# Optimization experiments

Measured on AMD Instinct MI355X. Metric: run time of the kernel, lower is better.

## Reference

```python
import jax, jax.numpy as jnp
import numpy as np

N, E = 50000, 1600000
IN, HID, OUT, H, ED = 128, 16, 40, 4, 16
HC = HID * H  # 64
NEG_SLOPE = 0.2
EPS = 1e-16


def gat_conv(x, src, dst, e_attr, W, att_s, att_d, We, att_e, bias):
    # x: [N, Fin]; src/dst: [E_tot]; e_attr: [E_tot, ED]
    n = x.shape[0]
    h = (x @ W).reshape(n, H, HID)                      # [N,H,C]
    a_s = (h * att_s).sum(-1)                           # [N,H]
    a_d = (h * att_d).sum(-1)                           # [N,H]
    ee = (e_attr @ We).reshape(-1, H, HID)              # [E,H,C]
    a_e = (ee * att_e).sum(-1)                          # [E,H]
    alpha = a_s[src] + a_d[dst] + a_e                   # [E,H]
    alpha = jax.nn.leaky_relu(alpha, NEG_SLOPE)
    amax = jax.ops.segment_max(alpha, dst, num_segments=n)
    ex = jnp.exp(alpha - amax[dst])
    den = jax.ops.segment_sum(ex, dst, num_segments=n)
    alpha = ex / (den[dst] + EPS)
    msg = h[src] * alpha[..., None]                     # [E,H,C]
    out = jax.ops.segment_sum(msg, dst, num_segments=n) # [N,H,C]
    return out.reshape(n, HC) + bias


def setup_inputs() -> dict:
    key = jax.random.key(0)
    ks = jax.random.split(key, 20)
    s = 0.05
    inp = {
        "x": jax.random.normal(ks[0], (N, IN), jnp.float32),
        "edge_index": jax.random.randint(ks[1], (2, E), 0, N, jnp.int64 if jax.config.jax_enable_x64 else jnp.int32),
        "edge_attr": jax.random.normal(ks[2], (E, ED), jnp.float32),
        # conv1
        "W1": jax.random.normal(ks[3], (IN, HC)) * s,
        "att_src1": jax.random.normal(ks[4], (H, HID)) * s,
        "att_dst1": jax.random.normal(ks[5], (H, HID)) * s,
        "We1": jax.random.normal(ks[6], (ED, HC)) * s,
        "att_e1": jax.random.normal(ks[7], (H, HID)) * s,
        "b1": jnp.zeros((HC,), jnp.float32),
        # conv2
        "W2": jax.random.normal(ks[8], (HC, HC)) * s,
        "att_src2": jax.random.normal(ks[9], (H, HID)) * s,
        "att_dst2": jax.random.normal(ks[10], (H, HID)) * s,
        "We2": jax.random.normal(ks[11], (ED, HC)) * s,
        "att_e2": jax.random.normal(ks[12], (H, HID)) * s,
        "b2": jnp.zeros((HC,), jnp.float32),
        # head
        "lw1": jax.random.normal(ks[13], (HC, HID)) * s,
        "lb1": jnp.zeros((HID,), jnp.float32),
        "lw2": jax.random.normal(ks[14], (HID, OUT)) * s,
        "lb2": jnp.zeros((OUT,), jnp.float32),
    }
    return inp


def reference(x, edge_index, edge_attr,
              W1, att_src1, att_dst1, We1, att_e1, b1,
              W2, att_src2, att_dst2, We2, att_e2, b2,
              lw1, lb1, lw2, lb2):
    n = x.shape[0]
    loop = jnp.arange(n, dtype=edge_index.dtype)
    src = jnp.concatenate([edge_index[0], loop])
    dst = jnp.concatenate([edge_index[1], loop])
    # self-loop edge_attr filled with mean over edges (PyG fill_value='mean')
    mean_attr = edge_attr.mean(axis=0, keepdims=True)
    ea = jnp.concatenate([edge_attr, jnp.broadcast_to(mean_attr, (n, edge_attr.shape[1]))])

    h = gat_conv(x, src, dst, ea, W1, att_src1, att_dst1, We1, att_e1, b1)
    h = jax.nn.relu(h)  # dropout is identity at eval
    h = gat_conv(h, src, dst, ea, W2, att_src2, att_dst2, We2, att_e2, b2)
    h = jax.nn.relu(h)
    h = (h @ lw1 + lb1) @ lw2 + lb2  # Linear -> Dropout(eval) -> Linear
    return jax.nn.log_softmax(h, axis=1)
```

## Files before the change

kernel.cpp:

```cpp
#include <hip/hip_runtime.h>
#include <hip/hip_fp16.h>

#define N_NODES 50000
#define E_EDGES 1600000
#define NEG 0.2f
#define EDGE_BLOCKS 6250
#define RED_BLOCKS 64
#define SCAN_BLOCKS ((N_NODES + 255)/256)
#define HBLK 128
#define EPHB (E_EDGES/HBLK)
#define NPAIR (N_NODES/2)
#define NODE_BLOCKS 2048

__device__ __forceinline__ float lrelu(float x){ return fmaxf(x, NEG*x); }
__device__ __forceinline__ float bcastlane(float v, int k){
    return __int_as_float(__builtin_amdgcn_readlane(__float_as_int(v), k));
}
__device__ __forceinline__ unsigned bf16rn(float x){
    unsigned u = __float_as_uint(x);
    return (u + 0x7FFFu + ((u >> 16) & 1u)) >> 16;
}
__device__ __forceinline__ float bf2f(unsigned short u){
    return __uint_as_float(((unsigned)u) << 16);
}
__device__ __forceinline__ unsigned h16(float x){
    return (unsigned)__half_as_ushort(__float2half(x));
}
__device__ __forceinline__ float f16dec(unsigned u){
    return __half2float(__ushort_as_half((unsigned short)(u & 0xFFFFu)));
}

#if __has_builtin(__builtin_amdgcn_cvt_f32_fp8) && __has_builtin(__builtin_amdgcn_cvt_pk_fp8_f32)
__device__ __forceinline__ unsigned enc8(float x){
    return (unsigned)__builtin_amdgcn_cvt_pk_fp8_f32(x, x, 0, false) & 0xFFu;
}
__device__ __forceinline__ float dec8(unsigned b){
    return __builtin_amdgcn_cvt_f32_fp8((int)b, 0);
}
#else
__device__ __forceinline__ unsigned enc8(float x){
    float ax = fabsf(x); unsigned s = (x < 0.f) ? 0x80u : 0u;
    if (ax < 0.015625f){
        int q = (int)rintf(ax * 512.f);
        return s | (unsigned)q;
    }
    if (ax >= 448.f) return s | 0x7Eu;
    int ee; float mm = frexpf(ax, &ee);
    int q = (int)rintf(mm * 16.f);
    int E = ee + 6;
    if (q == 16){ q = 8; ++E; }
    if (E > 15){ return s | 0x7Eu; }
    return s | ((unsigned)E << 3) | (unsigned)(q - 8);
}
__device__ __forceinline__ float dec8(unsigned b){
    unsigned s = b >> 7, e = (b >> 3) & 15u, m = b & 7u;
    float mag = e ? __uint_as_float(((e + 120u) << 23) | (m << 20))
                  : (float)m * 0.001953125f;
    return s ? -mag : mag;
}
#endif


__global__ void k_prep1(const float* __restrict__ We1, const float* __restrict__ atte1,
                        const float* __restrict__ We2, const float* __restrict__ atte2,
                        float* __restrict__ small){
    int t = threadIdx.x;
    int k = t >> 2, hh = t & 3;
    float w1 = 0.f, w2 = 0.f;
    for (int c = 0; c < 16; ++c){
        w1 = fmaf(We1[k*64 + hh*16 + c], atte1[hh*16 + c], w1);
        w2 = fmaf(We2[k*64 + hh*16 + c], atte2[hh*16 + c], w2);
    }
    small[32 + t] = w1;
    small[96 + t] = w2;
}

__global__ __launch_bounds__(256) void k_hist1(const int* __restrict__ dst,
                                               unsigned* __restrict__ bhist,
                                               unsigned short* __restrict__ lrank){
    extern __shared__ unsigned hist[];
    for (int i = threadIdx.x; i < NPAIR; i += 256) hist[i] = 0u;
    __syncthreads();
    int b0 = blockIdx.x*EPHB;
    for (int i = threadIdx.x; i < EPHB; i += 256){
        int e = b0 + i;
        int d = dst[e];
        unsigned sh = (unsigned)(d & 1) * 16u;
        unsigned old = atomicAdd(&hist[d >> 1], 1u << sh);
        lrank[e] = (unsigned short)((old >> sh) & 0xFFFFu);
    }
    __syncthreads();
    unsigned* bh = bhist + (size_t)blockIdx.x*NPAIR;
    for (int i = threadIdx.x; i < NPAIR; i += 256) bh[i] = hist[i];
}

__global__ __launch_bounds__(256) void k_hist2(const unsigned* __restrict__ bhist,
                                               unsigned* __restrict__ boff,
                                               int* __restrict__ deg){
    int j = blockIdx.x*256 + threadIdx.x;
    if (j >= NPAIR) return;
    unsigned lo = 0, hi = 0;
    for (int b = 0; b < HBLK; ++b){
        unsigned v = bhist[(size_t)b*NPAIR + j];
        boff[(size_t)b*NPAIR + j] = lo | (hi << 16);
        lo += v & 0xFFFFu;
        hi += v >> 16;
    }
    deg[2*j]     = (int)lo;
    deg[2*j + 1] = (int)hi;
}

__global__ __launch_bounds__(256) void k_scan_a(const int* __restrict__ deg, int* __restrict__ bsum){
    int i = blockIdx.x*256 + threadIdx.x;
    int v = (i < N_NODES) ? deg[i] : 0;
    v += __shfl_xor(v,1); v += __shfl_xor(v,2); v += __shfl_xor(v,4);
    v += __shfl_xor(v,8); v += __shfl_xor(v,16); v += __shfl_xor(v,32);
    __shared__ int ws[4];
    if ((threadIdx.x & 63) == 0) ws[threadIdx.x >> 6] = v;
    __syncthreads();
    if (threadIdx.x == 0) bsum[blockIdx.x] = ws[0] + ws[1] + ws[2] + ws[3];
}

__global__ __launch_bounds__(256) void k_scan_b(const int* __restrict__ bsum, int* __restrict__ boff){
    __shared__ int sm[256];
    int t = threadIdx.x;
    int v = (t < SCAN_BLOCKS) ? bsum[t] : 0;
    sm[t] = v;
    __syncthreads();
    for (int off = 1; off < 256; off <<= 1){
        int u = (t >= off) ? sm[t-off] : 0;
        __syncthreads();
        sm[t] += u;
        __syncthreads();
    }
    boff[t] = (t > 0) ? sm[t-1] : 0;
    if (t == 0) boff[SCAN_BLOCKS] = sm[255];
}

__global__ __launch_bounds__(256) void k_scan_c(const int* __restrict__ deg, const int* __restrict__ boff,
                                                int* __restrict__ base){
    int i = blockIdx.x*256 + threadIdx.x;
    int lane = threadIdx.x & 63, wid = threadIdx.x >> 6;
    int v = (i < N_NODES) ? deg[i] : 0;
    int inc = v;
    for (int off = 1; off < 64; off <<= 1){
        int u = __shfl_up(inc, off);
        if (lane >= off) inc += u;
    }
    __shared__ int wsum[4];
    if (lane == 63) wsum[wid] = inc;
    __syncthreads();
    int wpre = 0;
#pragma unroll
    for (int w = 0; w < 4; ++w) wpre += (w < wid) ? wsum[w] : 0;
    int ex = boff[blockIdx.x] + wpre + inc - v;
    if (i < N_NODES) base[i] = ex;
    if (i == N_NODES - 1) base[N_NODES] = ex + v;
}

template<int FIN>
__global__ __launch_bounds__(256) void k_node(const float* __restrict__ in, const float* __restrict__ W,
                                              const float* __restrict__ att_s, const float* __restrict__ att_d,
                                              unsigned char* __restrict__ hb8,
                                              unsigned short* __restrict__ a_s,
                                              unsigned short* __restrict__ a_d){
    __shared__ float Wl[FIN*64];
    for (int i = threadIdx.x; i < FIN*64; i += 256) Wl[i] = W[i];
    __syncthreads();
    int lane = threadIdx.x & 63;
    int wid  = threadIdx.x >> 6;
    for (int nb = blockIdx.x*4; nb < N_NODES; nb += NODE_BLOCKS*4){
        int node = nb + wid;
        const float* row = in + (size_t)node*FIN;
        float x0 = row[lane];
        float x1 = 0.f;
        if constexpr (FIN == 128) x1 = row[64 + lane];
        float acc = 0.f;
#pragma unroll
        for (int k = 0; k < 64; ++k)
            acc = fmaf(bcastlane(x0, k), Wl[k*64 + lane], acc);
        if constexpr (FIN == 128){
#pragma unroll
            for (int k = 0; k < 64; ++k)
                acc = fmaf(bcastlane(x1, k), Wl[(64+k)*64 + lane], acc);
        }
        hb8[(size_t)node*64 + lane] = (unsigned char)enc8(acc);
        float ps = acc * att_s[lane];
        float pd = acc * att_d[lane];
        ps += __shfl_xor(ps,1); ps += __shfl_xor(ps,2); ps += __shfl_xor(ps,4); ps += __shfl_xor(ps,8);
        pd += __shfl_xor(pd,1); pd += __shfl_xor(pd,2); pd += __shfl_xor(pd,4); pd += __shfl_xor(pd,8);
        if ((lane & 15) == 0){
            a_s[node*4 + (lane>>4)] = (unsigned short)bf16rn(ps);
            a_d[node*4 + (lane>>4)] = (unsigned short)bf16rn(pd);
        }
    }
}

__global__ __launch_bounds__(256) void k_edges(const int* __restrict__ src, const int* __restrict__ dst,
                                               const unsigned short* __restrict__ lrank,
                                               const unsigned* __restrict__ boff32,
                                               const float* __restrict__ ea, const float* __restrict__ small,
                                               const int* __restrict__ base, uint4* __restrict__ rec,
                                               float* __restrict__ partials){
    __shared__ float w1[64], w2[64];
    __shared__ float red[64];
    if (threadIdx.x < 64){ w1[threadIdx.x] = small[32+threadIdx.x]; w2[threadIdx.x] = small[96+threadIdx.x]; }
    __syncthreads();
    int e = blockIdx.x*256 + threadIdx.x;
    int s = src[e], d = dst[e];
    int hb = e / EPHB;
    unsigned offpk = boff32[(size_t)hb*NPAIR + (d >> 1)];
    int p = base[d] + (int)((offpk >> ((unsigned)(d & 1)*16u)) & 0xFFFFu) + (int)lrank[e];
    const float4* eap = (const float4*)(ea + (size_t)e*16);
    float cs[16];
    float ae1[4] = {0,0,0,0}, ae2[4] = {0,0,0,0};
#pragma unroll
    for (int q = 0; q < 4; ++q){
        float4 v4 = eap[q];
        float vv[4] = {v4.x, v4.y, v4.z, v4.w};
#pragma unroll
        for (int r = 0; r < 4; ++r){
            int k = q*4 + r;
            float xv = vv[r];
            cs[k] = xv;
#pragma unroll
            for (int hh = 0; hh < 4; ++hh){
                ae1[hh] = fmaf(xv, w1[k*4+hh], ae1[hh]);
                ae2[hh] = fmaf(xv, w2[k*4+hh], ae2[hh]);
            }
        }
    }
    unsigned q8[4];
#pragma unroll
    for (int hh = 0; hh < 4; ++hh){
        int qv = (int)rintf(ae2[hh]*256.f) + 128;
        qv = qv < 0 ? 0 : (qv > 255 ? 255 : qv);
        q8[hh] = (unsigned)qv;
    }
    uint4 r;
    r.x = (unsigned)s;
    r.y = h16(ae1[0]) | (h16(ae1[1]) << 16);
    r.z = h16(ae1[2]) | (h16(ae1[3]) << 16);
    r.w = q8[0] | (q8[1] << 8) | (q8[2] << 16) | (q8[3] << 24);
    rec[p] = r;
#pragma unroll
    for (int k = 0; k < 16; ++k){
        float v = cs[k];
        v += __shfl_xor(v,1); v += __shfl_xor(v,2); v += __shfl_xor(v,4);
        v += __shfl_xor(v,8); v += __shfl_xor(v,16); v += __shfl_xor(v,32);
        if ((threadIdx.x & 63) == 0) red[k*4 + (threadIdx.x>>6)] = v;
    }
    __syncthreads();
    if (threadIdx.x < 16){
        float v = red[threadIdx.x*4] + red[threadIdx.x*4+1] + red[threadIdx.x*4+2] + red[threadIdx.x*4+3];
        partials[blockIdx.x*16 + threadIdx.x] = v;
    }
}

__global__ __launch_bounds__(256) void k_red(const float* __restrict__ partials, float* __restrict__ red16){
    const int TOT = EDGE_BLOCKS*16;
    int t = threadIdx.x;
    float v = 0.f;
    for (int idx = blockIdx.x*256 + t; idx < TOT; idx += RED_BLOCKS*256) v += partials[idx];
    v += __shfl_xor(v,16); v += __shfl_xor(v,32);
    __shared__ float sm[64];
    int lane = t & 63, wid = t >> 6;
    if (lane < 16) sm[wid*16 + lane] = v;
    __syncthreads();
    if (t < 16) red16[blockIdx.x*16 + t] = sm[t] + sm[16+t] + sm[32+t] + sm[48+t];
}

__global__ __launch_bounds__(256) void k_prep2(float* __restrict__ small, const float* __restrict__ red16){
    __shared__ float sm[256];
    __shared__ float mean_s[16];
    int t = threadIdx.x;
    float v = 0.f;
    for (int r = (t>>4); r < RED_BLOCKS; r += 16) v += red16[r*16 + (t&15)];
    sm[t] = v;
    __syncthreads();
    if (t < 16){
        float s = 0.f;
#pragma unroll
        for (int i = 0; i < 16; ++i) s += sm[t + 16*i];
        float m = s * (1.0f/(float)E_EDGES);
        mean_s[t] = m; small[16+t] = m;
    }
    __syncthreads();
    if (t < 4){
        float a1 = 0.f, a2 = 0.f;
#pragma unroll
        for (int k = 0; k < 16; ++k){
            a1 = fmaf(mean_s[k], small[32 + k*4 + t], a1);
            a2 = fmaf(mean_s[k], small[96 + k*4 + t], a2);
        }
        small[160+t] = a1; small[164+t] = a2;
    }
}

template<int L>
__device__ __forceinline__ float ae_of(const uint4& r, int h4){
    if constexpr (L == 1){
        return f16dec(((h4 < 2) ? r.y : r.z) >> ((h4 & 1)*16));
    } else {
        return (float)((int)((r.w >> (h4*8)) & 255u) - 128) * 0.00390625f;
    }
}

template<int L>
__global__ __launch_bounds__(256) void k_agg(const uint4* __restrict__ recs, const int* __restrict__ base,
                                             const unsigned char* __restrict__ hb8,
                                             const unsigned short* __restrict__ a_s,
                                             const unsigned short* __restrict__ a_d,
                                             const float* __restrict__ aeloop, const float* __restrict__ bias,
                                             float* __restrict__ out){
    int lane = threadIdx.x & 63;
    int n = blockIdx.x*4 + (threadIdx.x >> 6);
    int hh = lane >> 4;
    int e16 = lane >> 2, h4 = lane & 3;
    float ad_acc = bf2f(a_d[n*4+hh]);
    float ad_w   = bf2f(a_d[n*4+h4]);
    float wL = __expf(lrelu(bf2f(a_s[n*4+hh]) + ad_acc + aeloop[hh]));
    float s0 = wL, s1 = 0.f, s2 = 0.f, s3 = 0.f;
    float acc0 = wL * dec8(hb8[(unsigned)n*64u + (unsigned)lane]);
    float acc1 = 0.f, acc2 = 0.f, acc3 = 0.f;
    int b0 = base[n], b1 = base[n+1];
    for (int pc = b0; pc < b1; pc += 32){
        int remA = b1 - pc;       int mA = remA < 16 ? remA : 16;
        int remB = b1 - pc - 16;  int mB = remB < 0 ? 0 : (remB < 16 ? remB : 16);
        float wa = 0.f, wb = 0.f;
        unsigned sia = 0u, sib = 0u;
        if (e16 < mA){
            uint4 r = recs[pc + e16];
            sia = r.x;
            wa = __expf(lrelu(bf2f(a_s[sia*4u + (unsigned)h4]) + ad_w + ae_of<L>(r, h4)));
        }
        if (e16 < mB){
            uint4 r = recs[pc + 16 + e16];
            sib = r.x;
            wb = __expf(lrelu(bf2f(a_s[sib*4u + (unsigned)h4]) + ad_w + ae_of<L>(r, h4)));
        }
        if (mA == 16){
#pragma unroll
            for (int j = 0; j < 16; j += 2){
                unsigned siA = (unsigned)__shfl((int)sia, j*4);
                unsigned siB = (unsigned)__shfl((int)sia, j*4 + 4);
                float wA = __shfl(wa, j*4 + hh);
                float wB = __shfl(wa, j*4 + 4 + hh);
                float hvA = dec8(hb8[siA*64u + (unsigned)lane]);
                float hvB = dec8(hb8[siB*64u + (unsigned)lane]);
                s0 += wA; acc0 = fmaf(wA, hvA, acc0);
                s1 += wB; acc1 = fmaf(wB, hvB, acc1);
            }
        } else {
            int j = 0;
            for (; j + 2 <= mA; j += 2){
                unsigned siA = (unsigned)__shfl((int)sia, j*4);
                unsigned siB = (unsigned)__shfl((int)sia, j*4 + 4);
                float wA = __shfl(wa, j*4 + hh);
                float wB = __shfl(wa, j*4 + 4 + hh);
                float hvA = dec8(hb8[siA*64u + (unsigned)lane]);
                float hvB = dec8(hb8[siB*64u + (unsigned)lane]);
                s0 += wA; acc0 = fmaf(wA, hvA, acc0);
                s1 += wB; acc1 = fmaf(wB, hvB, acc1);
            }
            if (j < mA){
                unsigned si = (unsigned)__shfl((int)sia, j*4);
                float wj = __shfl(wa, j*4 + hh);
                float hv = dec8(hb8[si*64u + (unsigned)lane]);
                s0 += wj; acc0 = fmaf(wj, hv, acc0);
            }
        }
        if (mB == 16){
#pragma unroll
            for (int j = 0; j < 16; j += 2){
                unsigned siA = (unsigned)__shfl((int)sib, j*4);
                unsigned siB = (unsigned)__shfl((int)sib, j*4 + 4);
                float wA = __shfl(wb, j*4 + hh);
                float wB = __shfl(wb, j*4 + 4 + hh);
                float hvA = dec8(hb8[siA*64u + (unsigned)lane]);
                float hvB = dec8(hb8[siB*64u + (unsigned)lane]);
                s2 += wA; acc2 = fmaf(wA, hvA, acc2);
                s3 += wB; acc3 = fmaf(wB, hvB, acc3);
            }
        } else if (mB > 0){
            int j = 0;
            for (; j + 2 <= mB; j += 2){
                unsigned siA = (unsigned)__shfl((int)sib, j*4);
                unsigned siB = (unsigned)__shfl((int)sib, j*4 + 4);
                float wA = __shfl(wb, j*4 + hh);
                float wB = __shfl(wb, j*4 + 4 + hh);
                float hvA = dec8(hb8[siA*64u + (unsigned)lane]);
                float hvB = dec8(hb8[siB*64u + (unsigned)lane]);
                s2 += wA; acc2 = fmaf(wA, hvA, acc2);
                s3 += wB; acc3 = fmaf(wB, hvB, acc3);
            }
            if (j < mB){
                unsigned si = (unsigned)__shfl((int)sib, j*4);
                float wj = __shfl(wb, j*4 + hh);
                float hv = dec8(hb8[si*64u + (unsigned)lane]);
                s2 += wj; acc2 = fmaf(wj, hv, acc2);
            }
        }
    }
    float s = (s0 + s1) + (s2 + s3);
    float val = ((acc0 + acc1) + (acc2 + acc3)) / (s + 1e-16f) + bias[lane];
    out[(size_t)n*64 + lane] = fmaxf(val, 0.f);
}

__global__ __launch_bounds__(256) void k_head(const float* __restrict__ h2,
                                              const float* __restrict__ lw1, const float* __restrict__ lb1,
                                              const float* __restrict__ lw2, const float* __restrict__ lb2,
                                              float* __restrict__ out){
    int n = blockIdx.x*256 + threadIdx.x;
    if (n >= N_NODES) return;
    float y16[16];
#pragma unroll
    for (int j = 0; j < 16; ++j) y16[j] = lb1[j];
    const float4* hp = (const float4*)(h2 + (size_t)n*64);
#pragma unroll
    for (int k4 = 0; k4 < 16; ++k4){
        float4 hv = hp[k4];
        float hvv[4] = {hv.x, hv.y, hv.z, hv.w};
#pragma unroll
        for (int r = 0; r < 4; ++r){
            float x = hvv[r];
            int k = k4*4 + r;
#pragma unroll
            for (int j = 0; j < 16; ++j) y16[j] = fmaf(x, lw1[k*16+j], y16[j]);
        }
    }
    float y[40];
#pragma unroll
    for (int o = 0; o < 40; ++o) y[o] = lb2[o];
#pragma unroll
    for (int j = 0; j < 16; ++j){
        float x = y16[j];
#pragma unroll
        for (int o = 0; o < 40; ++o) y[o] = fmaf(x, lw2[j*40+o], y[o]);
    }
    float mx = y[0];
#pragma unroll
    for (int o = 1; o < 40; ++o) mx = fmaxf(mx, y[o]);
    float sum = 0.f;
#pragma unroll
    for (int o = 0; o < 40; ++o) sum += __expf(y[o] - mx);
    float ls = __logf(sum) + mx;
    float* op = out + (size_t)n*40;
#pragma unroll
    for (int o = 0; o < 40; ++o) op[o] = y[o] - ls;
}

extern "C" void kernel_launch(void* const* d_in, const int* in_sizes, int n_in,
                              void* d_out, int out_size, void* d_ws, size_t ws_size,
                              hipStream_t stream){
    const float* x     = (const float*)d_in[0];
    const int*   ei    = (const int*)  d_in[1];
    const float* ea    = (const float*)d_in[2];
    const float* W1    = (const float*)d_in[3];
    const float* atts1 = (const float*)d_in[4];
    const float* attd1 = (const float*)d_in[5];
    const float* We1   = (const float*)d_in[6];
    const float* atte1 = (const float*)d_in[7];
    const float* b1    = (const float*)d_in[8];
    const float* W2    = (const float*)d_in[9];
    const float* atts2 = (const float*)d_in[10];
    const float* attd2 = (const float*)d_in[11];
    const float* We2   = (const float*)d_in[12];
    const float* atte2 = (const float*)d_in[13];
    const float* b2    = (const float*)d_in[14];
    const float* lw1   = (const float*)d_in[15];
    const float* lb1   = (const float*)d_in[16];
    const float* lw2   = (const float*)d_in[17];
    const float* lb2   = (const float*)d_in[18];
    float* outp = (float*)d_out;

    const int* srcp = ei;
    const int* dstp = ei + E_EDGES;

    char* ws = (char*)d_ws;
    size_t off = 0;
    auto alloc = [&](size_t bytes) -> void* {
        void* p = ws + off;
        off = (off + bytes + 255) & ~(size_t)255;
        return p;
    };
    float*  smallf   = (float*) alloc(256*sizeof(float));
    float*  partials = (float*) alloc((size_t)EDGE_BLOCKS*16*sizeof(float));
    float*  red16    = (float*) alloc((size_t)RED_BLOCKS*16*sizeof(float));
    int*    deg      = (int*)   alloc((size_t)N_NODES*sizeof(int));
    int*    base     = (int*)   alloc((size_t)(N_NODES+1)*sizeof(int));
    int*    bsum     = (int*)   alloc((size_t)(SCAN_BLOCKS+1)*sizeof(int));
    int*    boffs    = (int*)   alloc((size_t)(SCAN_BLOCKS+1)*sizeof(int));
    unsigned short* lrank = (unsigned short*)alloc((size_t)E_EDGES*sizeof(unsigned short));
    unsigned* bhist  = (unsigned*)alloc((size_t)HBLK*NPAIR*sizeof(unsigned));
    unsigned* boff32 = (unsigned*)alloc((size_t)HBLK*NPAIR*sizeof(unsigned));
    uint4*  rec      = (uint4*) alloc((size_t)E_EDGES*16);
    unsigned char* hb8 = (unsigned char*)alloc((size_t)N_NODES*64);
    float*  obuf     = (float*) alloc((size_t)N_NODES*64*sizeof(float));
    unsigned short* asb = (unsigned short*)alloc((size_t)N_NODES*4*sizeof(unsigned short));
    unsigned short* adb = (unsigned short*)alloc((size_t)N_NODES*4*sizeof(unsigned short));

    const int NB = N_NODES/4;
    const int HB = (N_NODES + 255)/256;
    const int PB = (NPAIR + 255)/256;

    k_prep1<<<1, 64, 0, stream>>>(We1, atte1, We2, atte2, smallf);
    k_hist1<<<HBLK, 256, NPAIR*sizeof(unsigned), stream>>>(dstp, bhist, lrank);
    k_hist2<<<PB, 256, 0, stream>>>(bhist, boff32, deg);
    k_scan_a<<<SCAN_BLOCKS, 256, 0, stream>>>(deg, bsum);
    k_scan_b<<<1, 256, 0, stream>>>(bsum, boffs);
    k_scan_c<<<SCAN_BLOCKS, 256, 0, stream>>>(deg, boffs, base);

    k_node<128><<<NODE_BLOCKS, 256, 0, stream>>>(x, W1, atts1, attd1, hb8, asb, adb);
    k_edges<<<EDGE_BLOCKS, 256, 0, stream>>>(srcp, dstp, lrank, boff32, ea, smallf,
                                             base, rec, partials);
    k_red<<<RED_BLOCKS, 256, 0, stream>>>(partials, red16);
    k_prep2<<<1, 256, 0, stream>>>(smallf, red16);
    k_agg<1><<<NB, 256, 0, stream>>>(rec, base, hb8, asb, adb, smallf + 160, b1, obuf);

    k_node<64><<<NODE_BLOCKS, 256, 0, stream>>>(obuf, W2, atts2, attd2, hb8, asb, adb);
    k_agg<2><<<NB, 256, 0, stream>>>(rec, base, hb8, asb, adb, smallf + 164, b2, obuf);

    k_head<<<HB, 256, 0, stream>>>(obuf, lw1, lb1, lw2, lb2, outp);
}
```

Before: 280.8 us.

## Fuse layer-2 node transform into agg1 and MLP head into agg2

The first aggregation kernel now computes the layer-2 linear projection and attention scores per node directly, using W2 staged in shared memory. The second aggregation fuses the head MLP and log-softmax, so the fp32 intermediate buffer and two extra launches go away. Both kernels switch to a fixed 2048-block grid-stride loop, which changes occupancy and scheduling. The edge-kernel reduction is also changed to reduce over 16-lane groups with a 256-entry shared buffer.

```diff
diff --git a/kernel.cpp b/kernel.cpp
--- a/kernel.cpp
+++ b/kernel.cpp
@@ -203,7 +203,7 @@
                                                const int* __restrict__ base, uint4* __restrict__ rec,
                                                float* __restrict__ partials){
     __shared__ float w1[64], w2[64];
-    __shared__ float red[64];
+    __shared__ float red[256];
     if (threadIdx.x < 64){ w1[threadIdx.x] = small[32+threadIdx.x]; w2[threadIdx.x] = small[96+threadIdx.x]; }
     __syncthreads();
     int e = blockIdx.x*256 + threadIdx.x;
@@ -246,13 +246,14 @@
 #pragma unroll
     for (int k = 0; k < 16; ++k){
         float v = cs[k];
-        v += __shfl_xor(v,1); v += __shfl_xor(v,2); v += __shfl_xor(v,4);
-        v += __shfl_xor(v,8); v += __shfl_xor(v,16); v += __shfl_xor(v,32);
-        if ((threadIdx.x & 63) == 0) red[k*4 + (threadIdx.x>>6)] = v;
+        v += __shfl_xor(v,1); v += __shfl_xor(v,2); v += __shfl_xor(v,4); v += __shfl_xor(v,8);
+        if ((threadIdx.x & 15) == k) red[k*16 + (threadIdx.x >> 4)] = v;
     }
     __syncthreads();
     if (threadIdx.x < 16){
-        float v = red[threadIdx.x*4] + red[threadIdx.x*4+1] + red[threadIdx.x*4+2] + red[threadIdx.x*4+3];
+        float v = 0.f;
+#pragma unroll
+        for (int g = 0; g < 16; ++g) v += red[threadIdx.x*16 + g];
         partials[blockIdx.x*16 + threadIdx.x] = v;
     }
 }
@@ -307,14 +308,13 @@
 }
 
 template<int L>
-__global__ __launch_bounds__(256) void k_agg(const uint4* __restrict__ recs, const int* __restrict__ base,
-                                             const unsigned char* __restrict__ hb8,
-                                             const unsigned short* __restrict__ a_s,
-                                             const unsigned short* __restrict__ a_d,
-                                             const float* __restrict__ aeloop, const float* __restrict__ bias,
-                                             float* __restrict__ out){
-    int lane = threadIdx.x & 63;
-    int n = blockIdx.x*4 + (threadIdx.x >> 6);
+__device__ __forceinline__ float agg_node(int n, int lane, const uint4* __restrict__ recs,
+                                          const int* __restrict__ base,
+                                          const unsigned char* __restrict__ hb8,
+                                          const unsigned short* __restrict__ a_s,
+                                          const unsigned short* __restrict__ a_d,
+                                          const float* __restrict__ aeloop,
+                                          const float* __restrict__ bias){
     int hh = lane >> 4;
     int e16 = lane >> 2, h4 = lane & 3;
     float ad_acc = bf2f(a_d[n*4+hh]);
@@ -404,50 +404,85 @@
     }
     float s = (s0 + s1) + (s2 + s3);
     float val = ((acc0 + acc1) + (acc2 + acc3)) / (s + 1e-16f) + bias[lane];
-    out[(size_t)n*64 + lane] = fmaxf(val, 0.f);
-}
-
-__global__ __launch_bounds__(256) void k_head(const float* __restrict__ h2,
+    return fmaxf(val, 0.f);
+}
+
+__global__ __launch_bounds__(256) void k_agg1(const uint4* __restrict__ recs, const int* __restrict__ base,
+                                              const unsigned char* __restrict__ hb8a,
+                                              const unsigned short* __restrict__ as1,
+                                              const unsigned short* __restrict__ ad1,
+                                              const float* __restrict__ aeloop, const float* __restrict__ b1,
+                                              const float* __restrict__ W2,
+                                              const float* __restrict__ atts2, const float* __restrict__ attd2,
+                                              unsigned char* __restrict__ hb8b,
+                                              unsigned short* __restrict__ as2,
+                                              unsigned short* __restrict__ ad2){
+    __shared__ float Wl[64*64];
+    for (int i = threadIdx.x; i < 64*64; i += 256) Wl[i] = W2[i];
+    __syncthreads();
+    int lane = threadIdx.x & 63;
+    int wid  = threadIdx.x >> 6;
+    for (int n0 = blockIdx.x*4; n0 < N_NODES; n0 += NODE_BLOCKS*4){
+        int n = n0 + wid;
+        float val = agg_node<1>(n, lane, recs, base, hb8a, as1, ad1, aeloop, b1);
+        float acc = 0.f;
+#pragma unroll
+        for (int k = 0; k < 64; ++k)
+            acc = fmaf(bcastlane(val, k), Wl[k*64 + lane], acc);
+        hb8b[(size_t)n*64 + lane] = (unsigned char)enc8(acc);
+        float ps = acc * atts2[lane];
+        float pd = acc * attd2[lane];
+        ps += __shfl_xor(ps,1); ps += __shfl_xor(ps,2); ps += __shfl_xor(ps,4); ps += __shfl_xor(ps,8);
+        pd += __shfl_xor(pd,1); pd += __shfl_xor(pd,2); pd += __shfl_xor(pd,4); pd += __shfl_xor(pd,8);
+        if ((lane & 15) == 0){
+            as2[n*4 + (lane>>4)] = (unsigned short)bf16rn(ps);
+            ad2[n*4 + (lane>>4)] = (unsigned short)bf16rn(pd);
+        }
+    }
+}
+
+__global__ __launch_bounds__(256) void k_agg2(const uint4* __restrict__ recs, const int* __restrict__ base,
+                                              const unsigned char* __restrict__ hb8b,
+                                              const unsigned short* __restrict__ as2,
+                                              const unsigned short* __restrict__ ad2,
+                                              const float* __restrict__ aeloop, const float* __restrict__ b2,
                                               const float* __restrict__ lw1, const float* __restrict__ lb1,
                                               const float* __restrict__ lw2, const float* __restrict__ lb2,
                                               float* __restrict__ out){
-    int n = blockIdx.x*256 + threadIdx.x;
-    if (n >= N_NODES) return;
-    float y16[16];
-#pragma unroll
-    for (int j = 0; j < 16; ++j) y16[j] = lb1[j];
-    const float4* hp = (const float4*)(h2 + (size_t)n*64);
-#pragma unroll
-    for (int k4 = 0; k4 < 16; ++k4){
-        float4 hv = hp[k4];
-        float hvv[4] = {hv.x, hv.y, hv.z, hv.w};
-#pragma unroll
-        for (int r = 0; r < 4; ++r){
-            float x = hvv[r];
-            int k = k4*4 + r;
-#pragma unroll
-            for (int j = 0; j < 16; ++j) y16[j] = fmaf(x, lw1[k*16+j], y16[j]);
-        }
-    }
-    float y[40];
-#pragma unroll
-    for (int o = 0; o < 40; ++o) y[o] = lb2[o];
-#pragma unroll
-    for (int j = 0; j < 16; ++j){
-        float x = y16[j];
-#pragma unroll
-        for (int o = 0; o < 40; ++o) y[o] = fmaf(x, lw2[j*40+o], y[o]);
-    }
-    float mx = y[0];
-#pragma unroll
-    for (int o = 1; o < 40; ++o) mx = fmaxf(mx, y[o]);
-    float sum = 0.f;
-#pragma unroll
-    for (int o = 0; o < 40; ++o) sum += __expf(y[o] - mx);
-    float ls = __logf(sum) + mx;
-    float* op = out + (size_t)n*40;
-#pragma unroll
-    for (int o = 0; o < 40; ++o) op[o] = y[o] - ls;
+    __shared__ float lw1s[64*16];
+    __shared__ float lw2s[16*40];
+    __shared__ float hsh[4][64];
+    __shared__ float ysh[4][16];
+    for (int i = threadIdx.x; i < 64*16; i += 256) lw1s[i] = lw1[i];
+    for (int i = threadIdx.x; i < 16*40; i += 256) lw2s[i] = lw2[i];
+    __syncthreads();
+    int lane = threadIdx.x & 63;
+    int wid  = threadIdx.x >> 6;
+    for (int n0 = blockIdx.x*4; n0 < N_NODES; n0 += NODE_BLOCKS*4){
+        int n = n0 + wid;
+        float val = agg_node<2>(n, lane, recs, base, hb8b, as2, ad2, aeloop, b2);
+        hsh[wid][lane] = val;
+        if (lane < 16){
+            float y = lb1[lane];
+#pragma unroll
+            for (int c = 0; c < 64; ++c) y = fmaf(hsh[wid][c], lw1s[c*16 + lane], y);
+            ysh[wid][lane] = y;
+        }
+        float yv = 0.f;
+        if (lane < 40){
+            yv = lb2[lane];
+#pragma unroll
+            for (int j = 0; j < 16; ++j) yv = fmaf(ysh[wid][j], lw2s[j*40 + lane], yv);
+        }
+        float m = (lane < 40) ? yv : -3.4e38f;
+        m = fmaxf(m, __shfl_xor(m,1)); m = fmaxf(m, __shfl_xor(m,2)); m = fmaxf(m, __shfl_xor(m,4));
+        m = fmaxf(m, __shfl_xor(m,8)); m = fmaxf(m, __shfl_xor(m,16)); m = fmaxf(m, __shfl_xor(m,32));
+        float ex = (lane < 40) ? __expf(yv - m) : 0.f;
+        ex += __shfl_xor(ex,1); ex += __shfl_xor(ex,2); ex += __shfl_xor(ex,4);
+        ex += __shfl_xor(ex,8); ex += __shfl_xor(ex,16); ex += __shfl_xor(ex,32);
+        float ls = __logf(ex) + m;
+        if (lane < 40) out[(size_t)n*40 + lane] = yv - ls;
+    }
 }
 
 extern "C" void kernel_launch(void* const* d_in, const int* in_sizes, int n_in,
@@ -495,13 +530,13 @@
     unsigned* bhist  = (unsigned*)alloc((size_t)HBLK*NPAIR*sizeof(unsigned));
     unsigned* boff32 = (unsigned*)alloc((size_t)HBLK*NPAIR*sizeof(unsigned));
     uint4*  rec      = (uint4*) alloc((size_t)E_EDGES*16);
-    unsigned char* hb8 = (unsigned char*)alloc((size_t)N_NODES*64);
-    float*  obuf     = (float*) alloc((size_t)N_NODES*64*sizeof(float));
-    unsigned short* asb = (unsigned short*)alloc((size_t)N_NODES*4*sizeof(unsigned short));
-    unsigned short* adb = (unsigned short*)alloc((size_t)N_NODES*4*sizeof(unsigned short));
-
-    const int NB = N_NODES/4;
-    const int HB = (N_NODES + 255)/256;
+    unsigned char* hb8a = (unsigned char*)alloc((size_t)N_NODES*64);
+    unsigned char* hb8b = (unsigned char*)alloc((size_t)N_NODES*64);
+    unsigned short* as1 = (unsigned short*)alloc((size_t)N_NODES*4*sizeof(unsigned short));
+    unsigned short* ad1 = (unsigned short*)alloc((size_t)N_NODES*4*sizeof(unsigned short));
+    unsigned short* as2 = (unsigned short*)alloc((size_t)N_NODES*4*sizeof(unsigned short));
+    unsigned short* ad2 = (unsigned short*)alloc((size_t)N_NODES*4*sizeof(unsigned short));
+
     const int PB = (NPAIR + 255)/256;
 
     k_prep1<<<1, 64, 0, stream>>>(We1, atte1, We2, atte2, smallf);
@@ -511,15 +546,15 @@
     k_scan_b<<<1, 256, 0, stream>>>(bsum, boffs);
     k_scan_c<<<SCAN_BLOCKS, 256, 0, stream>>>(deg, boffs, base);
 
-    k_node<128><<<NODE_BLOCKS, 256, 0, stream>>>(x, W1, atts1, attd1, hb8, asb, adb);
+    k_node<128><<<NODE_BLOCKS, 256, 0, stream>>>(x, W1, atts1, attd1, hb8a, as1, ad1);
     k_edges<<<EDGE_BLOCKS, 256, 0, stream>>>(srcp, dstp, lrank, boff32, ea, smallf,
                                              base, rec, partials);
     k_red<<<RED_BLOCKS, 256, 0, stream>>>(partials, red16);
     k_prep2<<<1, 256, 0, stream>>>(smallf, red16);
-    k_agg<1><<<NB, 256, 0, stream>>>(rec, base, hb8, asb, adb, smallf + 160, b1, obuf);
-
-    k_node<64><<<NODE_BLOCKS, 256, 0, stream>>>(obuf, W2, atts2, attd2, hb8, asb, adb);
-    k_agg<2><<<NB, 256, 0, stream>>>(rec, base, hb8, asb, adb, smallf + 164, b2, obuf);
-
-    k_head<<<HB, 256, 0, stream>>>(obuf, lw1, lb1, lw2, lb2, outp);
-}
+
+    k_agg1<<<NODE_BLOCKS, 256, 0, stream>>>(rec, base, hb8a, as1, ad1, smallf + 160, b1,
+                                            W2, atts2, attd2, hb8b, as2, ad2);
+
+    k_agg2<<<NODE_BLOCKS, 256, 0, stream>>>(rec, base, hb8b, as2, ad2, smallf + 164, b2,
+                                            lw1, lb1, lw2, lb2, outp);
+}
```

After: 353.0 us. +25.7%, slower.
